# Performance work log

Measured on AMD Instinct MI355X. Metric: run time of the kernel, lower is better.

## Reference

```python
import jax, jax.numpy as jnp
import numpy as np

B, S, H = 32, 8, 4096          # batch, new tokens, hidden
HQ, HK, D, L = 32, 8, 128, 4096  # q heads, kv heads, head_dim, max cache len
HALF = D // 2
W_STD = 0.02


def setup_inputs() -> dict:
    key = jax.random.key(0)
    ks = jax.random.split(key, 8)
    hidden_states = jax.random.normal(ks[0], (B, S, H), jnp.float32)
    past_key_value = jax.random.normal(ks[1], (2, B, L, HK, D), jnp.float32)
    rope_rotary_cos_sin = jax.random.uniform(ks[2], (B, S, 2, HALF), jnp.float32)
    context_lengths = jax.random.randint(ks[3], (B,), 0, L - S, dtype=jnp.int32)
    kvcache_start_index = context_lengths  # new tokens appended right after context
    Wq = jax.random.normal(ks[4], (HQ * D, H), jnp.float32) * W_STD
    Wk = jax.random.normal(ks[5], (HK * D, H), jnp.float32) * W_STD
    Wv = jax.random.normal(ks[6], (HK * D, H), jnp.float32) * W_STD
    Wo = jax.random.normal(ks[7], (H, HQ * D), jnp.float32) * W_STD
    return {
        'hidden_states': hidden_states,
        'past_key_value': past_key_value,
        'rope_rotary_cos_sin': rope_rotary_cos_sin,
        'context_lengths': context_lengths,
        'kvcache_start_index': kvcache_start_index,
        'Wq': Wq, 'Wk': Wk, 'Wv': Wv, 'Wo': Wo,
    }


def reference(hidden_states, past_key_value, rope_rotary_cos_sin,
              context_lengths, kvcache_start_index, Wq, Wk, Wv, Wo):
    # q/k/v projections (no bias)
    q = (hidden_states @ Wq.T).reshape(B, S, HQ, D)
    k = (hidden_states @ Wk.T).reshape(B, S, HK, D)
    v = (hidden_states @ Wv.T).reshape(B, S, HK, D)

    # inline RoPE (rotate-half, GPT-NeoX style) on q and k
    cos = rope_rotary_cos_sin[:, :, 0][:, :, None, :]  # [B,S,1,HALF]
    sin = rope_rotary_cos_sin[:, :, 1][:, :, None, :]

    def rot(x):
        x1, x2 = x[..., :HALF], x[..., HALF:]
        return jnp.concatenate([x1 * cos - x2 * sin, x2 * cos + x1 * sin], axis=-1)

    q = rot(q)
    k = rot(k)

    # write new k/v into the cache at kvcache_start_index (ragged per batch)
    b_idx = jnp.arange(B)[:, None]                                # [B,1]
    pos = kvcache_start_index[:, None] + jnp.arange(S)[None, :]   # [B,S]
    k_cache = past_key_value[0].at[b_idx, pos].set(k)             # [B,L,HK,D]
    v_cache = past_key_value[1].at[b_idx, pos].set(v)
    present_key_value = jnp.stack([k_cache, v_cache])

    # GQA attention: group 4 query heads per kv head
    G = HQ // HK
    qg = q.reshape(B, S, HK, G, D)
    scale = 1.0 / jnp.sqrt(jnp.asarray(D, q.dtype))
    scores = jnp.einsum('bshgd,blhd->bhgsl', qg, k_cache) * scale  # [B,HK,G,S,L]

    # causal mask over ragged context: key j visible iff j <= ctx_len + t
    q_pos = context_lengths[:, None, None] + jnp.arange(S)[None, :, None]  # [B,S,1]
    valid = jnp.arange(L)[None, None, :] <= q_pos                          # [B,S,L]
    scores = jnp.where(valid[:, None, None, :, :], scores,
                       jnp.finfo(scores.dtype).min)
    probs = jax.nn.softmax(scores, axis=-1)
    attn = jnp.einsum('bhgsl,blhd->bshgd', probs, v_cache).reshape(B, S, HQ * D)

    return attn @ Wo.T, present_key_value
```

## Files before the change

### kernel.cpp

```cpp
#include <hip/hip_runtime.h>

#define B_ 32
#define S_ 8
#define H_ 4096
#define HQ_ 32
#define HK_ 8
#define D_ 128
#define L_ 4096
#define KK 4096

typedef short s16x8 __attribute__((ext_vector_type(8)));
typedef float f32x4 __attribute__((ext_vector_type(4)));

static __device__ __forceinline__ unsigned short f2bf(float x){
  unsigned int u = __builtin_bit_cast(unsigned int, x);
  u += 0x7fffu + ((u >> 16) & 1u);
  return (unsigned short)(u >> 16);
}

static __device__ __forceinline__ s16x8 cvt8(f32x4 a, f32x4 b){
  s16x8 r;
  r[0]=(short)f2bf(a[0]); r[1]=(short)f2bf(a[1]); r[2]=(short)f2bf(a[2]); r[3]=(short)f2bf(a[3]);
  r[4]=(short)f2bf(b[0]); r[5]=(short)f2bf(b[1]); r[6]=(short)f2bf(b[2]); r[7]=(short)f2bf(b[3]);
  return r;
}

__global__ __launch_bounds__(256) void gemm_qkv(const float* __restrict__ A,
    const float* __restrict__ Wq, const float* __restrict__ Wk,
    const float* __restrict__ Wv, float* __restrict__ C)
{
  __shared__ short As[64][72];
  __shared__ short Bs[64][72];
  const int m0 = blockIdx.y * 64;
  const int n0 = blockIdx.x * 64;
  const float* W; int nw;
  if (n0 < 4096){ W = Wq; nw = n0; }
  else if (n0 < 5120){ W = Wk; nw = n0 - 4096; }
  else { W = Wv; nw = n0 - 5120; }
  const int tid = threadIdx.x;
  const int lane = tid & 63;
  const int w = tid >> 6;
  const int c = lane & 15;
  const int g = lane >> 4;
  const int wm = (w & 1) * 32;
  const int wn = (w >> 1) * 32;
  const int srow = tid >> 3;
  const int skc  = tid & 7;

  const float* Ar0 = A + (m0 + srow) * KK + skc * 8;
  const float* Ar1 = Ar0 + 32 * KK;
  const float* Wr0 = W + (nw + srow) * KK + skc * 8;
  const float* Wr1 = Wr0 + 32 * KK;

  f32x4 acc00 = {0.f,0.f,0.f,0.f};
  f32x4 acc01 = acc00, acc10 = acc00, acc11 = acc00;

  for (int kt = 0; kt < KK; kt += 64){
    __syncthreads();
    {
      f32x4 x0 = *(const f32x4*)(Ar0 + kt);
      f32x4 x1 = *(const f32x4*)(Ar0 + kt + 4);
      f32x4 x2 = *(const f32x4*)(Ar1 + kt);
      f32x4 x3 = *(const f32x4*)(Ar1 + kt + 4);
      f32x4 y0 = *(const f32x4*)(Wr0 + kt);
      f32x4 y1 = *(const f32x4*)(Wr0 + kt + 4);
      f32x4 y2 = *(const f32x4*)(Wr1 + kt);
      f32x4 y3 = *(const f32x4*)(Wr1 + kt + 4);
      *(s16x8*)&As[srow][skc*8]    = cvt8(x0, x1);
      *(s16x8*)&As[srow+32][skc*8] = cvt8(x2, x3);
      *(s16x8*)&Bs[srow][skc*8]    = cvt8(y0, y1);
      *(s16x8*)&Bs[srow+32][skc*8] = cvt8(y2, y3);
    }
    __syncthreads();
#pragma unroll
    for (int kk = 0; kk < 2; ++kk){
      s16x8 a0 = *(const s16x8*)&As[wm + c][kk*32 + 8*g];
      s16x8 a1 = *(const s16x8*)&As[wm + 16 + c][kk*32 + 8*g];
      s16x8 b0 = *(const s16x8*)&Bs[wn + c][kk*32 + 8*g];
      s16x8 b1 = *(const s16x8*)&Bs[wn + 16 + c][kk*32 + 8*g];
      acc00 = __builtin_amdgcn_mfma_f32_16x16x32_bf16(a0, b0, acc00, 0, 0, 0);
      acc01 = __builtin_amdgcn_mfma_f32_16x16x32_bf16(a0, b1, acc01, 0, 0, 0);
      acc10 = __builtin_amdgcn_mfma_f32_16x16x32_bf16(a1, b0, acc10, 0, 0, 0);
      acc11 = __builtin_amdgcn_mfma_f32_16x16x32_bf16(a1, b1, acc11, 0, 0, 0);
    }
  }
#pragma unroll
  for (int r = 0; r < 4; ++r){
    int row0 = m0 + wm + 4*g + r;
    int row1 = row0 + 16;
    int col0 = n0 + wn + c;
    int col1 = col0 + 16;
    C[row0 * 6144 + col0] = acc00[r];
    C[row0 * 6144 + col1] = acc01[r];
    C[row1 * 6144 + col0] = acc10[r];
    C[row1 * 6144 + col1] = acc11[r];
  }
}

__global__ __launch_bounds__(256) void gemm_bt(const float* __restrict__ A,
    const float* __restrict__ W, float* __restrict__ C, int N)
{
  __shared__ short As[64][72];
  __shared__ short Bs[64][72];
  const int m0 = blockIdx.y * 64;
  const int n0 = blockIdx.x * 64;
  const int tid = threadIdx.x;
  const int lane = tid & 63;
  const int w = tid >> 6;
  const int c = lane & 15;
  const int g = lane >> 4;
  const int wm = (w & 1) * 32;
  const int wn = (w >> 1) * 32;
  const int srow = tid >> 3;
  const int skc  = tid & 7;

  const float* Ar0 = A + (m0 + srow) * KK + skc * 8;
  const float* Ar1 = Ar0 + 32 * KK;
  const float* Wr0 = W + (n0 + srow) * KK + skc * 8;
  const float* Wr1 = Wr0 + 32 * KK;

  f32x4 acc00 = {0.f,0.f,0.f,0.f};
  f32x4 acc01 = acc00, acc10 = acc00, acc11 = acc00;

  for (int kt = 0; kt < KK; kt += 64){
    __syncthreads();
    {
      f32x4 x0 = *(const f32x4*)(Ar0 + kt);
      f32x4 x1 = *(const f32x4*)(Ar0 + kt + 4);
      f32x4 x2 = *(const f32x4*)(Ar1 + kt);
      f32x4 x3 = *(const f32x4*)(Ar1 + kt + 4);
      f32x4 y0 = *(const f32x4*)(Wr0 + kt);
      f32x4 y1 = *(const f32x4*)(Wr0 + kt + 4);
      f32x4 y2 = *(const f32x4*)(Wr1 + kt);
      f32x4 y3 = *(const f32x4*)(Wr1 + kt + 4);
      *(s16x8*)&As[srow][skc*8]    = cvt8(x0, x1);
      *(s16x8*)&As[srow+32][skc*8] = cvt8(x2, x3);
      *(s16x8*)&Bs[srow][skc*8]    = cvt8(y0, y1);
      *(s16x8*)&Bs[srow+32][skc*8] = cvt8(y2, y3);
    }
    __syncthreads();
#pragma unroll
    for (int kk = 0; kk < 2; ++kk){
      s16x8 a0 = *(const s16x8*)&As[wm + c][kk*32 + 8*g];
      s16x8 a1 = *(const s16x8*)&As[wm + 16 + c][kk*32 + 8*g];
      s16x8 b0 = *(const s16x8*)&Bs[wn + c][kk*32 + 8*g];
      s16x8 b1 = *(const s16x8*)&Bs[wn + 16 + c][kk*32 + 8*g];
      acc00 = __builtin_amdgcn_mfma_f32_16x16x32_bf16(a0, b0, acc00, 0, 0, 0);
      acc01 = __builtin_amdgcn_mfma_f32_16x16x32_bf16(a0, b1, acc01, 0, 0, 0);
      acc10 = __builtin_amdgcn_mfma_f32_16x16x32_bf16(a1, b0, acc10, 0, 0, 0);
      acc11 = __builtin_amdgcn_mfma_f32_16x16x32_bf16(a1, b1, acc11, 0, 0, 0);
    }
  }
#pragma unroll
  for (int r = 0; r < 4; ++r){
    int row0 = m0 + wm + 4*g + r;
    int row1 = row0 + 16;
    int col0 = n0 + wn + c;
    int col1 = col0 + 16;
    C[row0 * N + col0] = acc00[r];
    C[row0 * N + col1] = acc01[r];
    C[row1 * N + col0] = acc10[r];
    C[row1 * N + col1] = acc11[r];
  }
}

__global__ __launch_bounds__(256) void rope_prep(
    const float* __restrict__ qkv, const float* __restrict__ rope,
    unsigned short* __restrict__ qbuf, float* __restrict__ wskr, float* __restrict__ wsvc)
{
  const int bs = blockIdx.x;
  const int tid = threadIdx.x;
  const float* cosv = rope + bs * 128;
  const float* sinv = cosv + 64;
  const float* row = qkv + bs * 6144;
#pragma unroll
  for (int it = 0; it < 16; ++it){
    int e = tid + it * 256;
    int d = e & 127; int dh = d & 63;
    float x  = row[e];
    float xp = row[e ^ 64];
    float o = (d < 64) ? (x * cosv[dh] - xp * sinv[dh]) : (x * cosv[dh] + xp * sinv[dh]);
    qbuf[bs*4096 + e] = f2bf(o);
  }
#pragma unroll
  for (int it = 0; it < 4; ++it){
    int e = tid + it * 256;
    int d = e & 127; int dh = d & 63;
    float x  = row[4096 + e];
    float xp = row[4096 + (e ^ 64)];
    float o = (d < 64) ? (x * cosv[dh] - xp * sinv[dh]) : (x * cosv[dh] + xp * sinv[dh]);
    wskr[bs*1024 + e] = o;
    wsvc[bs*1024 + e] = row[5120 + e];
  }
}

template<bool FAST>
static __device__ __forceinline__ void attn_chunk(
    int l0, int ctx, int pos,
    const float* __restrict__ Kpast, const float* __restrict__ Vpast,
    const float* __restrict__ KnewB, const float* __restrict__ VnewB,
    float* __restrict__ Kout, float* __restrict__ Vout,
    const s16x8 (&qf)[2][4], f32x4 (&accO)[2][8],
    float (&m_j)[2], float (&s_j)[2],
    int c, int g)
{
  const float scale = 0.08838834764831845f;
  f32x4 zero4 = {0.f,0.f,0.f,0.f};

  s16x8 kf[2][4];
#pragma unroll
  for (int i = 0; i < 2; ++i){
    int row = l0 + i*16 + c;
    const float* src;
    if (FAST){
      src = Kpast + row*1024 + 8*g;
    } else {
      bool kn = ((unsigned)(row - pos)) < 8u;
      src = (kn ? KnewB : Kpast) + row*1024 + 8*g;
    }
    float* dst = Kout + row*1024 + 8*g;
#pragma unroll
    for (int ks = 0; ks < 4; ++ks){
      f32x4 x = *(const f32x4*)(src + ks*32);
      f32x4 y = *(const f32x4*)(src + ks*32 + 4);
      __builtin_nontemporal_store(x, (f32x4*)(dst + ks*32));
      __builtin_nontemporal_store(y, (f32x4*)(dst + ks*32 + 4));
      kf[i][ks] = cvt8(x, y);
    }
  }
  f32x4 sc[2][2];
#pragma unroll
  for (int i = 0; i < 2; ++i)
#pragma unroll
    for (int j = 0; j < 2; ++j) sc[i][j] = zero4;
#pragma unroll
  for (int ks = 0; ks < 4; ++ks)
#pragma unroll
    for (int i = 0; i < 2; ++i)
#pragma unroll
      for (int j = 0; j < 2; ++j)
        sc[i][j] = __builtin_amdgcn_mfma_f32_16x16x32_bf16(kf[i][ks], qf[j][ks], sc[i][j], 0, 0, 0);

  float p[2][2][4];
  float fj[2];
#pragma unroll
  for (int j = 0; j < 2; ++j){
    const int qpos = ctx + ((j*16 + c) & 7);
    float mx = -1e30f;
#pragma unroll
    for (int i = 0; i < 2; ++i)
#pragma unroll
      for (int r = 0; r < 4; ++r){
        float v;
        if (FAST){
          v = sc[i][j][r] * scale;
        } else {
          int lg = l0 + i*16 + 4*g + r;
          v = (lg <= qpos) ? sc[i][j][r] * scale : -1e30f;
        }
        p[i][j][r] = v;
        mx = fmaxf(mx, v);
      }
    mx = fmaxf(mx, __shfl_xor(mx, 16));
    mx = fmaxf(mx, __shfl_xor(mx, 32));
    float mnew = fmaxf(m_j[j], mx);
    float f = __expf(m_j[j] - mnew);
    float lsum = 0.f;
#pragma unroll
    for (int i = 0; i < 2; ++i)
#pragma unroll
      for (int r = 0; r < 4; ++r){
        float pv;
        if (FAST){
          pv = __expf(p[i][j][r] - mnew);
        } else {
          int lg = l0 + i*16 + 4*g + r;
          pv = (lg <= qpos) ? __expf(p[i][j][r] - mnew) : 0.f;
        }
        p[i][j][r] = pv;
        lsum += pv;
      }
    s_j[j] = s_j[j] * f + lsum;
    m_j[j] = mnew;
    fj[j] = f;
  }
#pragma unroll
  for (int iq = 0; iq < 2; ++iq)
#pragma unroll
    for (int r = 0; r < 4; ++r){
      float fo = __shfl(fj[iq], 4*g + r);
#pragma unroll
      for (int t = 0; t < 8; ++t) accO[iq][t][r] *= fo;
    }
  s16x8 pf[2];
#pragma unroll
  for (int iq = 0; iq < 2; ++iq){
    int pd00 = (int)((unsigned)f2bf(p[0][iq][0]) | ((unsigned)f2bf(p[0][iq][1]) << 16));
    int pd01 = (int)((unsigned)f2bf(p[0][iq][2]) | ((unsigned)f2bf(p[0][iq][3]) << 16));
    int pd10 = (int)((unsigned)f2bf(p[1][iq][0]) | ((unsigned)f2bf(p[1][iq][1]) << 16));
    int pd11 = (int)((unsigned)f2bf(p[1][iq][2]) | ((unsigned)f2bf(p[1][iq][3]) << 16));
    int sA = (((2*g) & 3) << 4) | c;
    int sB = (((2*g + 1) & 3) << 4) | c;
    int h = g >> 1;
    int t0a = __shfl(pd00, sA), t1a = __shfl(pd10, sA);
    int t0b = __shfl(pd01, sA), t1b = __shfl(pd11, sA);
    int t0c = __shfl(pd00, sB), t1c = __shfl(pd10, sB);
    int t0d = __shfl(pd01, sB), t1d = __shfl(pd11, sB);
    int4 dw;
    dw.x = h ? t1a : t0a;
    dw.y = h ? t1b : t0b;
    dw.z = h ? t1c : t0c;
    dw.w = h ? t1d : t0d;
    pf[iq] = __builtin_bit_cast(s16x8, dw);
  }
#pragma unroll
  for (int t = 0; t < 8; ++t){
    const int co = t*16 + c;
    float vv[8];
#pragma unroll
    for (int jj = 0; jj < 8; ++jj){
      int row = l0 + 8*g + jj;
      float x;
      if (FAST){
        x = Vpast[row*1024 + co];
      } else {
        bool kn = ((unsigned)(row - pos)) < 8u;
        x = *((kn ? VnewB : Vpast) + row*1024 + co);
      }
      __builtin_nontemporal_store(x, Vout + row*1024 + co);
      vv[jj] = x;
    }
    f32x4 va, vb;
    va[0] = vv[0]; va[1] = vv[1]; va[2] = vv[2]; va[3] = vv[3];
    vb[0] = vv[4]; vb[1] = vv[5]; vb[2] = vv[6]; vb[3] = vv[7];
    s16x8 vf = cvt8(va, vb);
    accO[0][t] = __builtin_amdgcn_mfma_f32_16x16x32_bf16(pf[0], vf, accO[0][t], 0, 0, 0);
    accO[1][t] = __builtin_amdgcn_mfma_f32_16x16x32_bf16(pf[1], vf, accO[1][t], 0, 0, 0);
  }
}

__global__ __launch_bounds__(256) void copy_attn(
    const float* __restrict__ past, const float* __restrict__ wskr,
    const float* __restrict__ wsvc, const unsigned short* __restrict__ qb,
    const int* __restrict__ ctxlen, const int* __restrict__ startv,
    float* __restrict__ cache,
    float* __restrict__ pO, float* __restrict__ pM, float* __restrict__ pS)
{
  const int bid = blockIdx.x;
  const int sp = bid & 3;
  const int hk = (bid >> 2) & 7;
  const int b  = bid >> 5;
  const int tid = threadIdx.x;
  const int w = tid >> 6;
  const int lane = tid & 63;
  const int c = lane & 15;
  const int g = lane >> 4;
  const int ctx = ctxlen[b];
  const int pos = startv[b];
  const int lbase = sp * 1024;
  const int pid = bid * 4 + w;

  const float* Kpast = past + (size_t)b * 4194304 + hk * 128;
  const float* Vpast = Kpast + 134217728;
  float* Kout = cache + (size_t)b * 4194304 + hk * 128;
  float* Vout = Kout + 134217728;
  const float* KnewB = wskr + b * 8192 + hk * 128 - pos * 1024;
  const float* VnewB = wsvc + b * 8192 + hk * 128 - pos * 1024;

  s16x8 qf[2][4];
#pragma unroll
  for (int j = 0; j < 2; ++j){
    int r = j*16 + c; int s = r & 7; int gh = r >> 3;
    const unsigned short* qp = qb + (((b*8 + s) * 32) + hk*4 + gh) * 128 + 8*g;
#pragma unroll
    for (int ks = 0; ks < 4; ++ks)
      qf[j][ks] = __builtin_bit_cast(s16x8, *(const uint4*)(qp + ks*32));
  }

  f32x4 zero4 = {0.f,0.f,0.f,0.f};
  f32x4 accO[2][8];
#pragma unroll
  for (int i = 0; i < 2; ++i)
#pragma unroll
    for (int t = 0; t < 8; ++t) accO[i][t] = zero4;

  float m_j[2] = {-1e30f, -1e30f};
  float s_j[2] = {0.f, 0.f};

  const int rr = lane >> 5;
  const int fq = lane & 31;

  int attLim = 0;
  {
    int t1 = ctx + 7 - lbase;
    if (t1 >= 0){ attLim = (t1 >> 5) + 1; if (attLim > 32) attLim = 32; }
  }

  for (int ci = w; ci < attLim; ci += 4){
    const int l0 = lbase + ci * 32;
    bool fullValid = (l0 + 31 <= ctx);
    bool hasNew = (l0 <= pos + 7) && (l0 + 31 >= pos);
    if (fullValid && !hasNew)
      attn_chunk<true >(l0, ctx, pos, Kpast, Vpast, KnewB, VnewB, Kout, Vout,
                        qf, accO, m_j, s_j, c, g);
    else
      attn_chunk<false>(l0, ctx, pos, Kpast, Vpast, KnewB, VnewB, Kout, Vout,
                        qf, accO, m_j, s_j, c, g);
  }

  int st2 = attLim + (((w - attLim) % 4) + 4) % 4;
  for (int ci = st2; ci < 32; ci += 4){
    const int l0 = lbase + ci * 32;
    bool hasNew = (l0 <= pos + 7) && (l0 + 31 >= pos);
    if (!hasNew){
#pragma unroll
      for (int j = 0; j < 16; ++j){
        int row = l0 + rr + 2*j;
        const f32x4* kp = (const f32x4*)(Kpast + row*1024) + fq;
        const f32x4* vp = (const f32x4*)(Vpast + row*1024) + fq;
        f32x4 kv = __builtin_nontemporal_load(kp);
        f32x4 vv = __builtin_nontemporal_load(vp);
        __builtin_nontemporal_store(kv, (f32x4*)(Kout + row*1024) + fq);
        __builtin_nontemporal_store(vv, (f32x4*)(Vout + row*1024) + fq);
      }
    } else {
#pragma unroll
      for (int j = 0; j < 16; ++j){
        int row = l0 + rr + 2*j;
        bool kn = ((unsigned)(row - pos)) < 8u;
        const f32x4* kp = (const f32x4*)((kn ? KnewB : Kpast) + row*1024) + fq;
        const f32x4* vp = (const f32x4*)((kn ? VnewB : Vpast) + row*1024) + fq;
        f32x4 kv = __builtin_nontemporal_load(kp);
        f32x4 vv = __builtin_nontemporal_load(vp);
        __builtin_nontemporal_store(kv, (f32x4*)(Kout + row*1024) + fq);
        __builtin_nontemporal_store(vv, (f32x4*)(Vout + row*1024) + fq);
      }
    }
  }

#pragma unroll
  for (int j = 0; j < 2; ++j){
    float sj = s_j[j];
    sj += __shfl_xor(sj, 16);
    sj += __shfl_xor(sj, 32);
    if (g == 0){
      pM[pid*32 + j*16 + c] = m_j[j];
      pS[pid*32 + j*16 + c] = sj;
    }
  }
#pragma unroll
  for (int iq = 0; iq < 2; ++iq)
#pragma unroll
    for (int t = 0; t < 8; ++t)
#pragma unroll
      for (int r = 0; r < 4; ++r)
        pO[(pid*32 + iq*16 + 4*g + r) * 128 + t*16 + c] = accO[iq][t][r];
}

__global__ __launch_bounds__(256) void merge_attn(const float* __restrict__ pO,
    const float* __restrict__ pM, const float* __restrict__ pS, float* __restrict__ attn)
{
  const int bh = blockIdx.x;
  const int b = bh >> 3, hk = bh & 7;
  const int tid = threadIdx.x;
  const int q = tid >> 3;
  const int d0 = (tid & 7) * 16;
  const int base = bh * 16;
  float eP[16];
  float M = -1e30f;
#pragma unroll
  for (int p2 = 0; p2 < 16; ++p2){
    float m = pM[(base + p2) * 32 + q];
    eP[p2] = m;
    M = fmaxf(M, m);
  }
  float den = 0.f;
#pragma unroll
  for (int p2 = 0; p2 < 16; ++p2){
    float e = __expf(eP[p2] - M);
    eP[p2] = e;
    den += e * pS[(base + p2) * 32 + q];
  }
  float inv = 1.f / den;
  float a[16];
#pragma unroll
  for (int k2 = 0; k2 < 16; ++k2) a[k2] = 0.f;
#pragma unroll
  for (int p2 = 0; p2 < 16; ++p2){
    const float* src = pO + ((base + p2) * 32 + q) * 128 + d0;
    float e = eP[p2];
    f32x4 v0 = *(const f32x4*)(src);
    f32x4 v1 = *(const f32x4*)(src + 4);
    f32x4 v2 = *(const f32x4*)(src + 8);
    f32x4 v3 = *(const f32x4*)(src + 12);
    a[0]  += e * v0[0]; a[1]  += e * v0[1]; a[2]  += e * v0[2]; a[3]  += e * v0[3];
    a[4]  += e * v1[0]; a[5]  += e * v1[1]; a[6]  += e * v1[2]; a[7]  += e * v1[3];
    a[8]  += e * v2[0]; a[9]  += e * v2[1]; a[10] += e * v2[2]; a[11] += e * v2[3];
    a[12] += e * v3[0]; a[13] += e * v3[1]; a[14] += e * v3[2]; a[15] += e * v3[3];
  }
  const int gh = q >> 3, s = q & 7;
  float* o = attn + (b*8 + s) * 4096 + (hk*4 + gh) * 128 + d0;
#pragma unroll
  for (int k2 = 0; k2 < 16; ++k2) o[k2] = a[k2] * inv;
}

extern "C" void kernel_launch(void* const* d_in, const int* in_sizes, int n_in,
                              void* d_out, int out_size, void* d_ws, size_t ws_size,
                              hipStream_t stream) {
  const float* hidden = (const float*)d_in[0];
  const float* past   = (const float*)d_in[1];
  const float* rope   = (const float*)d_in[2];
  const int*   ctx    = (const int*)d_in[3];
  const int*   start  = (const int*)d_in[4];
  const float* Wq     = (const float*)d_in[5];
  const float* Wk     = (const float*)d_in[6];
  const float* Wv     = (const float*)d_in[7];
  const float* Wo     = (const float*)d_in[8];

  float* out_attn  = (float*)d_out;
  float* out_cache = out_attn + 1048576;

  float* ws = (float*)d_ws;
  float* qkv    = ws;
  float* wsattn = ws + 1572864;
  float* wskr   = wsattn;
  float* wsvc   = wsattn + 262144;
  unsigned short* qb = (unsigned short*)(ws + 2621440);
  float* pO = ws + 3145728;
  float* pM = ws + 19922944;
  float* pS = ws + 20054016;

  gemm_qkv<<<dim3(96, 4), 256, 0, stream>>>(hidden, Wq, Wk, Wv, qkv);

  rope_prep<<<256, 256, 0, stream>>>(qkv, rope, qb, wskr, wsvc);

  copy_attn<<<1024, 256, 0, stream>>>(past, wskr, wsvc, qb, ctx, start,
                                      out_cache, pO, pM, pS);
  merge_attn<<<B_ * HK_, 256, 0, stream>>>(pO, pM, pS, wsattn);

  gemm_bt<<<dim3(64, 4), 256, 0, stream>>>(wsattn, Wo, out_attn, 4096);
}
```

Baseline: 718.3 us.

## Overlap KV cache copy of unattended rows with QKV GEMM in one launch

New measurement: 839.0 us. 1.17x slower.

```diff
diff --git a/kernel.cpp b/kernel.cpp
--- a/kernel.cpp
+++ b/kernel.cpp
@@ -25,75 +25,126 @@
   return r;
 }
 
-__global__ __launch_bounds__(256) void gemm_qkv(const float* __restrict__ A,
-    const float* __restrict__ Wq, const float* __restrict__ Wk,
-    const float* __restrict__ Wv, float* __restrict__ C)
+__global__ __launch_bounds__(256) void qkv_copy(
+    const float* __restrict__ A, const float* __restrict__ Wq,
+    const float* __restrict__ Wk, const float* __restrict__ Wv,
+    float* __restrict__ C,
+    const float* __restrict__ past, float* __restrict__ cache,
+    const int* __restrict__ ctxlen, const int* __restrict__ startv)
 {
-  __shared__ short As[64][72];
-  __shared__ short Bs[64][72];
-  const int m0 = blockIdx.y * 64;
-  const int n0 = blockIdx.x * 64;
-  const float* W; int nw;
-  if (n0 < 4096){ W = Wq; nw = n0; }
-  else if (n0 < 5120){ W = Wk; nw = n0 - 4096; }
-  else { W = Wv; nw = n0 - 5120; }
   const int tid = threadIdx.x;
+  if (blockIdx.x < 384){
+    __shared__ short As[64][72];
+    __shared__ short Bs[64][72];
+    const int m0 = (blockIdx.x & 3) * 64;
+    const int n0 = (blockIdx.x >> 2) * 64;
+    const float* W; int nw;
+    if (n0 < 4096){ W = Wq; nw = n0; }
+    else if (n0 < 5120){ W = Wk; nw = n0 - 4096; }
+    else { W = Wv; nw = n0 - 5120; }
+    const int lane = tid & 63;
+    const int w = tid >> 6;
+    const int c = lane & 15;
+    const int g = lane >> 4;
+    const int wm = (w & 1) * 32;
+    const int wn = (w >> 1) * 32;
+    const int srow = tid >> 3;
+    const int skc  = tid & 7;
+
+    const float* Ar0 = A + (m0 + srow) * KK + skc * 8;
+    const float* Ar1 = Ar0 + 32 * KK;
+    const float* Wr0 = W + (nw + srow) * KK + skc * 8;
+    const float* Wr1 = Wr0 + 32 * KK;
+
+    f32x4 acc00 = {0.f,0.f,0.f,0.f};
+    f32x4 acc01 = acc00, acc10 = acc00, acc11 = acc00;
+
+    for (int kt = 0; kt < KK; kt += 64){
+      __syncthreads();
+      {
+        f32x4 x0 = *(const f32x4*)(Ar0 + kt);
+        f32x4 x1 = *(const f32x4*)(Ar0 + kt + 4);
+        f32x4 x2 = *(const f32x4*)(Ar1 + kt);
+        f32x4 x3 = *(const f32x4*)(Ar1 + kt + 4);
+        f32x4 y0 = *(const f32x4*)(Wr0 + kt);
+        f32x4 y1 = *(const f32x4*)(Wr0 + kt + 4);
+        f32x4 y2 = *(const f32x4*)(Wr1 + kt);
+        f32x4 y3 = *(const f32x4*)(Wr1 + kt + 4);
+        *(s16x8*)&As[srow][skc*8]    = cvt8(x0, x1);
+        *(s16x8*)&As[srow+32][skc*8] = cvt8(x2, x3);
+        *(s16x8*)&Bs[srow][skc*8]    = cvt8(y0, y1);
+        *(s16x8*)&Bs[srow+32][skc*8] = cvt8(y2, y3);
+      }
+      __syncthreads();
+#pragma unroll
+      for (int kk = 0; kk < 2; ++kk){
+        s16x8 a0 = *(const s16x8*)&As[wm + c][kk*32 + 8*g];
+        s16x8 a1 = *(const s16x8*)&As[wm + 16 + c][kk*32 + 8*g];
+        s16x8 b0 = *(const s16x8*)&Bs[wn + c][kk*32 + 8*g];
+        s16x8 b1 = *(const s16x8*)&Bs[wn + 16 + c][kk*32 + 8*g];
+        acc00 = __builtin_amdgcn_mfma_f32_16x16x32_bf16(a0, b0, acc00, 0, 0, 0);
+        acc01 = __builtin_amdgcn_mfma_f32_16x16x32_bf16(a0, b1, acc01, 0, 0, 0);
+        acc10 = __builtin_amdgcn_mfma_f32_16x16x32_bf16(a1, b0, acc10, 0, 0, 0);
+        acc11 = __builtin_amdgcn_mfma_f32_16x16x32_bf16(a1, b1, acc11, 0, 0, 0);
+      }
+    }
+#pragma unroll
+    for (int r = 0; r < 4; ++r){
+      int row0 = m0 + wm + 4*g + r;
+      int row1 = row0 + 16;
+      int col0 = n0 + wn + c;
+      int col1 = col0 + 16;
+      C[row0 * 6144 + col0] = acc00[r];
+      C[row0 * 6144 + col1] = acc01[r];
+      C[row1 * 6144 + col0] = acc10[r];
+      C[row1 * 6144 + col1] = acc11[r];
+    }
+    return;
+  }
+  const int cid = blockIdx.x - 384;
+  const int sp = cid & 3;
+  const int hk = (cid >> 2) & 7;
+  const int b  = cid >> 5;
+  const int w = tid >> 6;
   const int lane = tid & 63;
-  const int w = tid >> 6;
-  const int c = lane & 15;
-  const int g = lane >> 4;
-  const int wm = (w & 1) * 32;
-  const int wn = (w >> 1) * 32;
-  const int srow = tid >> 3;
-  const int skc  = tid & 7;
-
-  const float* Ar0 = A + (m0 + srow) * KK + skc * 8;
-  const float* Ar1 = Ar0 + 32 * KK;
-  const float* Wr0 = W + (nw + srow) * KK + skc * 8;
-  const float* Wr1 = Wr0 + 32 * KK;
-
-  f32x4 acc00 = {0.f,0.f,0.f,0.f};
-  f32x4 acc01 = acc00, acc10 = acc00, acc11 = acc00;
-
-  for (int kt = 0; kt < KK; kt += 64){
-    __syncthreads();
-    {
-      f32x4 x0 = *(const f32x4*)(Ar0 + kt);
-      f32x4 x1 = *(const f32x4*)(Ar0 + kt + 4);
-      f32x4 x2 = *(const f32x4*)(Ar1 + kt);
-      f32x4 x3 = *(const f32x4*)(Ar1 + kt + 4);
-      f32x4 y0 = *(const f32x4*)(Wr0 + kt);
-      f32x4 y1 = *(const f32x4*)(Wr0 + kt + 4);
-      f32x4 y2 = *(const f32x4*)(Wr1 + kt);
-      f32x4 y3 = *(const f32x4*)(Wr1 + kt + 4);
-      *(s16x8*)&As[srow][skc*8]    = cvt8(x0, x1);
-      *(s16x8*)&As[srow+32][skc*8] = cvt8(x2, x3);
-      *(s16x8*)&Bs[srow][skc*8]    = cvt8(y0, y1);
-      *(s16x8*)&Bs[srow+32][skc*8] = cvt8(y2, y3);
-    }
-    __syncthreads();
-#pragma unroll
-    for (int kk = 0; kk < 2; ++kk){
-      s16x8 a0 = *(const s16x8*)&As[wm + c][kk*32 + 8*g];
-      s16x8 a1 = *(const s16x8*)&As[wm + 16 + c][kk*32 + 8*g];
-      s16x8 b0 = *(const s16x8*)&Bs[wn + c][kk*32 + 8*g];
-      s16x8 b1 = *(const s16x8*)&Bs[wn + 16 + c][kk*32 + 8*g];
-      acc00 = __builtin_amdgcn_mfma_f32_16x16x32_bf16(a0, b0, acc00, 0, 0, 0);
-      acc01 = __builtin_amdgcn_mfma_f32_16x16x32_bf16(a0, b1, acc01, 0, 0, 0);
-      acc10 = __builtin_amdgcn_mfma_f32_16x16x32_bf16(a1, b0, acc10, 0, 0, 0);
-      acc11 = __builtin_amdgcn_mfma_f32_16x16x32_bf16(a1, b1, acc11, 0, 0, 0);
-    }
-  }
-#pragma unroll
-  for (int r = 0; r < 4; ++r){
-    int row0 = m0 + wm + 4*g + r;
-    int row1 = row0 + 16;
-    int col0 = n0 + wn + c;
-    int col1 = col0 + 16;
-    C[row0 * 6144 + col0] = acc00[r];
-    C[row0 * 6144 + col1] = acc01[r];
-    C[row1 * 6144 + col0] = acc10[r];
-    C[row1 * 6144 + col1] = acc11[r];
+  const int ctx = ctxlen[b];
+  const int pos = startv[b];
+  const int lbase = sp * 1024;
+  const float* Kpast = past + (size_t)b * 4194304 + hk * 128;
+  const float* Vpast = Kpast + 134217728;
+  float* Kout = cache + (size_t)b * 4194304 + hk * 128;
+  float* Vout = Kout + 134217728;
+  const int rr = lane >> 5;
+  const int fq = lane & 31;
+
+  int attLim = 0;
+  {
+    int t1 = ctx + 7 - lbase;
+    if (t1 >= 0){ attLim = (t1 >> 5) + 1; if (attLim > 32) attLim = 32; }
+  }
+  for (int ci = attLim + w; ci < 32; ci += 4){
+    const int l0 = lbase + ci * 32;
+    bool inter = (l0 <= pos + 7) && (l0 + 31 >= pos);
+    if (!inter){
+#pragma unroll
+      for (int j = 0; j < 16; ++j){
+        int row = l0 + rr + 2*j;
+        f32x4 kv = __builtin_nontemporal_load((const f32x4*)(Kpast + row*1024) + fq);
+        f32x4 vv = __builtin_nontemporal_load((const f32x4*)(Vpast + row*1024) + fq);
+        __builtin_nontemporal_store(kv, (f32x4*)(Kout + row*1024) + fq);
+        __builtin_nontemporal_store(vv, (f32x4*)(Vout + row*1024) + fq);
+      }
+    } else {
+      for (int j = 0; j < 16; ++j){
+        int row = l0 + rr + 2*j;
+        if (((unsigned)(row - pos)) >= 8u){
+          f32x4 kv = __builtin_nontemporal_load((const f32x4*)(Kpast + row*1024) + fq);
+          f32x4 vv = __builtin_nontemporal_load((const f32x4*)(Vpast + row*1024) + fq);
+          __builtin_nontemporal_store(kv, (f32x4*)(Kout + row*1024) + fq);
+          __builtin_nontemporal_store(vv, (f32x4*)(Vout + row*1024) + fq);
+        }
+      }
+    }
   }
 }
 
@@ -166,9 +217,13 @@
 
 __global__ __launch_bounds__(256) void rope_prep(
     const float* __restrict__ qkv, const float* __restrict__ rope,
-    unsigned short* __restrict__ qbuf, float* __restrict__ wskr, float* __restrict__ wsvc)
+    const int* __restrict__ startv,
+    unsigned short* __restrict__ qbuf, float* __restrict__ wskr,
+    float* __restrict__ wsvc, float* __restrict__ cache)
 {
   const int bs = blockIdx.x;
+  const int b = bs >> 3;
+  const int s = bs & 7;
   const int tid = threadIdx.x;
   const float* cosv = rope + bs * 128;
   const float* sinv = cosv + 64;
@@ -182,6 +237,9 @@
     float o = (d < 64) ? (x * cosv[dh] - xp * sinv[dh]) : (x * cosv[dh] + xp * sinv[dh]);
     qbuf[bs*4096 + e] = f2bf(o);
   }
+  const int pos = startv[b] + s;
+  float* kout = cache + ((size_t)b * 4096 + pos) * 1024;
+  float* vout = kout + 134217728;
 #pragma unroll
   for (int it = 0; it < 4; ++it){
     int e = tid + it * 256;
@@ -189,8 +247,11 @@
     float x  = row[4096 + e];
     float xp = row[4096 + (e ^ 64)];
     float o = (d < 64) ? (x * cosv[dh] - xp * sinv[dh]) : (x * cosv[dh] + xp * sinv[dh]);
+    float v = row[5120 + e];
     wskr[bs*1024 + e] = o;
-    wsvc[bs*1024 + e] = row[5120 + e];
+    wsvc[bs*1024 + e] = v;
+    kout[e] = o;
+    vout[e] = v;
   }
 }
 
@@ -360,82 +421,58 @@
   const int lbase = sp * 1024;
   const int pid = bid * 4 + w;
 
-  const float* Kpast = past + (size_t)b * 4194304 + hk * 128;
-  const float* Vpast = Kpast + 134217728;
-  float* Kout = cache + (size_t)b * 4194304 + hk * 128;
-  float* Vout = Kout + 134217728;
-  const float* KnewB = wskr + b * 8192 + hk * 128 - pos * 1024;
-  const float* VnewB = wsvc + b * 8192 + hk * 128 - pos * 1024;
-
-  s16x8 qf[2][4];
-#pragma unroll
-  for (int j = 0; j < 2; ++j){
-    int r = j*16 + c; int s = r & 7; int gh = r >> 3;
-    const unsigned short* qp = qb + (((b*8 + s) * 32) + hk*4 + gh) * 128 + 8*g;
-#pragma unroll
-    for (int ks = 0; ks < 4; ++ks)
-      qf[j][ks] = __builtin_bit_cast(s16x8, *(const uint4*)(qp + ks*32));
-  }
-
-  f32x4 zero4 = {0.f,0.f,0.f,0.f};
-  f32x4 accO[2][8];
-#pragma unroll
-  for (int i = 0; i < 2; ++i)
-#pragma unroll
-    for (int t = 0; t < 8; ++t) accO[i][t] = zero4;
-
-  float m_j[2] = {-1e30f, -1e30f};
-  float s_j[2] = {0.f, 0.f};
-
-  const int rr = lane >> 5;
-  const int fq = lane & 31;
-
   int attLim = 0;
   {
     int t1 = ctx + 7 - lbase;
     if (t1 >= 0){ attLim = (t1 >> 5) + 1; if (attLim > 32) attLim = 32; }
   }
 
-  for (int ci = w; ci < attLim; ci += 4){
-    const int l0 = lbase + ci * 32;
-    bool fullValid = (l0 + 31 <= ctx);
-    bool hasNew = (l0 <= pos + 7) && (l0 + 31 >= pos);
-    if (fullValid && !hasNew)
-      attn_chunk<true >(l0, ctx, pos, Kpast, Vpast, KnewB, VnewB, Kout, Vout,
-                        qf, accO, m_j, s_j, c, g);
-    else
-      attn_chunk<false>(l0, ctx, pos, Kpast, Vpast, KnewB, VnewB, Kout, Vout,
-                        qf, accO, m_j, s_j, c, g);
-  }
-
-  int st2 = attLim + (((w - attLim) % 4) + 4) % 4;
-  for (int ci = st2; ci < 32; ci += 4){
-    const int l0 = lbase + ci * 32;
-    bool hasNew = (l0 <= pos + 7) && (l0 + 31 >= pos);
-    if (!hasNew){
-#pragma unroll
-      for (int j = 0; j < 16; ++j){
-        int row = l0 + rr + 2*j;
-        const f32x4* kp = (const f32x4*)(Kpast + row*1024) + fq;
-        const f32x4* vp = (const f32x4*)(Vpast + row*1024) + fq;
-        f32x4 kv = __builtin_nontemporal_load(kp);
-        f32x4 vv = __builtin_nontemporal_load(vp);
-        __builtin_nontemporal_store(kv, (f32x4*)(Kout + row*1024) + fq);
-        __builtin_nontemporal_store(vv, (f32x4*)(Vout + row*1024) + fq);
-      }
-    } else {
-#pragma unroll
-      for (int j = 0; j < 16; ++j){
-        int row = l0 + rr + 2*j;
-        bool kn = ((unsigned)(row - pos)) < 8u;
-        const f32x4* kp = (const f32x4*)((kn ? KnewB : Kpast) + row*1024) + fq;
-        const f32x4* vp = (const f32x4*)((kn ? VnewB : Vpast) + row*1024) + fq;
-        f32x4 kv = __builtin_nontemporal_load(kp);
-        f32x4 vv = __builtin_nontemporal_load(vp);
-        __builtin_nontemporal_store(kv, (f32x4*)(Kout + row*1024) + fq);
-        __builtin_nontemporal_store(vv, (f32x4*)(Vout + row*1024) + fq);
-      }
-    }
+  f32x4 zero4 = {0.f,0.f,0.f,0.f};
+  float m_j[2] = {-1e30f, -1e30f};
+  float s_j[2] = {0.f, 0.f};
+
+  if (attLim > w){
+    const float* Kpast = past + (size_t)b * 4194304 + hk * 128;
+    const float* Vpast = Kpast + 134217728;
+    float* Kout = cache + (size_t)b * 4194304 + hk * 128;
+    float* Vout = Kout + 134217728;
+    const float* KnewB = wskr + b * 8192 + hk * 128 - pos * 1024;
+    const float* VnewB = wsvc + b * 8192 + hk * 128 - pos * 1024;
+
+    s16x8 qf[2][4];
+#pragma unroll
+    for (int j = 0; j < 2; ++j){
+      int r = j*16 + c; int s = r & 7; int gh = r >> 3;
+      const unsigned short* qp = qb + (((b*8 + s) * 32) + hk*4 + gh) * 128 + 8*g;
+#pragma unroll
+      for (int ks = 0; ks < 4; ++ks)
+        qf[j][ks] = __builtin_bit_cast(s16x8, *(const uint4*)(qp + ks*32));
+    }
+
+    f32x4 accO[2][8];
+#pragma unroll
+    for (int i = 0; i < 2; ++i)
+#pragma unroll
+      for (int t = 0; t < 8; ++t) accO[i][t] = zero4;
+
+    for (int ci = w; ci < attLim; ci += 4){
+      const int l0 = lbase + ci * 32;
+      bool fullValid = (l0 + 31 <= ctx);
+      bool hasNew = (l0 <= pos + 7) && (l0 + 31 >= pos);
+      if (fullValid && !hasNew)
+        attn_chunk<true >(l0, ctx, pos, Kpast, Vpast, KnewB, VnewB, Kout, Vout,
+                          qf, accO, m_j, s_j, c, g);
+      else
+        attn_chunk<false>(l0, ctx, pos, Kpast, Vpast, KnewB, VnewB, Kout, Vout,
+                          qf, accO, m_j, s_j, c, g);
+    }
+#pragma unroll
+    for (int iq = 0; iq < 2; ++iq)
+#pragma unroll
+      for (int t = 0; t < 8; ++t)
+#pragma unroll
+        for (int r = 0; r < 4; ++r)
+          pO[(pid*32 + iq*16 + 4*g + r) * 128 + t*16 + c] = accO[iq][t][r];
   }
 
 #pragma unroll
@@ -448,13 +485,6 @@
       pS[pid*32 + j*16 + c] = sj;
     }
   }
-#pragma unroll
-  for (int iq = 0; iq < 2; ++iq)
-#pragma unroll
-    for (int t = 0; t < 8; ++t)
-#pragma unroll
-      for (int r = 0; r < 4; ++r)
-        pO[(pid*32 + iq*16 + 4*g + r) * 128 + t*16 + c] = accO[iq][t][r];
 }
 
 __global__ __launch_bounds__(256) void merge_attn(const float* __restrict__ pO,
@@ -466,7 +496,7 @@
   const int q = tid >> 3;
   const int d0 = (tid & 7) * 16;
   const int base = bh * 16;
-  float eP[16];
+  float eP[16], sv[16];
   float M = -1e30f;
 #pragma unroll
   for (int p2 = 0; p2 < 16; ++p2){
@@ -477,9 +507,11 @@
   float den = 0.f;
 #pragma unroll
   for (int p2 = 0; p2 < 16; ++p2){
+    float s_ = pS[(base + p2) * 32 + q];
+    sv[p2] = s_;
     float e = __expf(eP[p2] - M);
     eP[p2] = e;
-    den += e * pS[(base + p2) * 32 + q];
+    den += e * s_;
   }
   float inv = 1.f / den;
   float a[16];
@@ -487,16 +519,18 @@
   for (int k2 = 0; k2 < 16; ++k2) a[k2] = 0.f;
 #pragma unroll
   for (int p2 = 0; p2 < 16; ++p2){
-    const float* src = pO + ((base + p2) * 32 + q) * 128 + d0;
-    float e = eP[p2];
-    f32x4 v0 = *(const f32x4*)(src);
-    f32x4 v1 = *(const f32x4*)(src + 4);
-    f32x4 v2 = *(const f32x4*)(src + 8);
-    f32x4 v3 = *(const f32x4*)(src + 12);
-    a[0]  += e * v0[0]; a[1]  += e * v0[1]; a[2]  += e * v0[2]; a[3]  += e * v0[3];
-    a[4]  += e * v1[0]; a[5]  += e * v1[1]; a[6]  += e * v1[2]; a[7]  += e * v1[3];
-    a[8]  += e * v2[0]; a[9]  += e * v2[1]; a[10] += e * v2[2]; a[11] += e * v2[3];
-    a[12] += e * v3[0]; a[13] += e * v3[1]; a[14] += e * v3[2]; a[15] += e * v3[3];
+    if (sv[p2] != 0.f){
+      const float* src = pO + ((base + p2) * 32 + q) * 128 + d0;
+      float e = eP[p2];
+      f32x4 v0 = *(const f32x4*)(src);
+      f32x4 v1 = *(const f32x4*)(src + 4);
+      f32x4 v2 = *(const f32x4*)(src + 8);
+      f32x4 v3 = *(const f32x4*)(src + 12);
+      a[0]  += e * v0[0]; a[1]  += e * v0[1]; a[2]  += e * v0[2]; a[3]  += e * v0[3];
+      a[4]  += e * v1[0]; a[5]  += e * v1[1]; a[6]  += e * v1[2]; a[7]  += e * v1[3];
+      a[8]  += e * v2[0]; a[9]  += e * v2[1]; a[10] += e * v2[2]; a[11] += e * v2[3];
+      a[12] += e * v3[0]; a[13] += e * v3[1]; a[14] += e * v3[2]; a[15] += e * v3[3];
+    }
   }
   const int gh = q >> 3, s = q & 7;
   float* o = attn + (b*8 + s) * 4096 + (hk*4 + gh) * 128 + d0;
@@ -530,9 +564,10 @@
   float* pM = ws + 19922944;
   float* pS = ws + 20054016;
 
-  gemm_qkv<<<dim3(96, 4), 256, 0, stream>>>(hidden, Wq, Wk, Wv, qkv);
-
-  rope_prep<<<256, 256, 0, stream>>>(qkv, rope, qb, wskr, wsvc);
+  qkv_copy<<<1408, 256, 0, stream>>>(hidden, Wq, Wk, Wv, qkv,
+                                     past, out_cache, ctx, start);
+
+  rope_prep<<<256, 256, 0, stream>>>(qkv, rope, start, qb, wskr, wsvc, out_cache);
 
   copy_attn<<<1024, 256, 0, stream>>>(past, wskr, wsvc, qb, ctx, start,
                                       out_cache, pO, pM, pS);
```
